# Performance work log

Measured on AMD Instinct MI355X. Metric: run time of the kernel, lower is better.

## Reference

```python
import jax, jax.numpy as jnp
import numpy as np

NUM_HEADS = 16
WINDOW_SIZE = 256  # config.window_size; layer is 'local'


def setup_inputs() -> dict:
    key = jax.random.key(0)
    ks = jax.random.split(key, 8)
    B, S, H = 4, 2048, 1024
    scale = 1.0 / np.sqrt(H)
    return {
        "x": jax.random.normal(ks[0], (B, S, H), dtype=jnp.float32),
        "x_clean": jax.random.normal(ks[1], (B, S, H), dtype=jnp.float32),
        "ablation_mask": jax.random.uniform(ks[2], (B, S, H), dtype=jnp.float32),
        "Wq": jax.random.normal(ks[3], (H, H), dtype=jnp.float32) * scale,
        "Wk": jax.random.normal(ks[4], (H, H), dtype=jnp.float32) * scale,
        "Wv": jax.random.normal(ks[5], (H, H), dtype=jnp.float32) * scale,
        "Wo": jax.random.normal(ks[6], (H, H), dtype=jnp.float32) * scale,
        "bo": jnp.zeros((H,), dtype=jnp.float32),
    }


def reference(x, x_clean, ablation_mask, Wq, Wk, Wv, Wo, bo):
    B, S, H = x.shape
    nh, hd = NUM_HEADS, H // NUM_HEADS

    def proj(inp, W):  # torch Linear: inp @ W.T -> split heads -> [B, nh, S, hd]
        return jnp.einsum('bsh,oh->bso', inp, W).reshape(B, S, nh, hd).transpose(0, 2, 1, 3)

    q = proj(x, Wq)
    k = proj(x_clean, Wk)
    v = proj(x_clean, Wv)

    # NOTE: original applies NO 1/sqrt(head_dim) scaling.
    scores = jnp.einsum('bnsd,bntd->bnst', q, k)  # [B, nh, S, S]

    i = jnp.arange(S)[:, None]
    j = jnp.arange(S)[None, :]
    # local mask: forbid future (j > i) OR too-far past (j <= i - window)
    masked = (j > i) | (j <= i - WINDOW_SIZE)
    scores = jnp.where(masked[None, None, :, :], -jnp.inf, scores)

    attn = jax.nn.softmax(scores, axis=-1)
    context = jnp.einsum('bnst,bntd->bnsd', attn, v)          # [B, nh, S, hd]
    context = context.transpose(0, 2, 1, 3).reshape(B, S, H)   # merge heads
    context = context * ablation_mask
    return jnp.einsum('bsh,oh->bso', context, Wo) + bo
```

## Files before the change

### kernel.cpp

```cpp
#include <hip/hip_runtime.h>
#include <hip/hip_bf16.h>
#include <cstddef>

#define SB 4
#define SS 2048
#define SH 1024
#define NH 16
#define HD 64
#define WIN 256

typedef __attribute__((ext_vector_type(8))) short bf16x8;
typedef __attribute__((ext_vector_type(8))) _Float16 f16x8;
typedef __attribute__((ext_vector_type(2))) __fp16 fp16v2;
typedef __attribute__((ext_vector_type(4))) float f32x4;

static __device__ __forceinline__ ushort2 pk_bf16(float a, float b) {
    __hip_bfloat162 h = __float22bfloat162_rn(make_float2(a, b));
    union { __hip_bfloat162 h2; ushort2 u2; } u;
    u.h2 = h;
    return u.u2;
}
static __device__ __forceinline__ unsigned short pk1(float a) {
    return pk_bf16(a, 0.f).x;
}

static __device__ __forceinline__ void async16(const void* gptr, void* lptr) {
    __builtin_amdgcn_global_load_lds(
        (const __attribute__((address_space(1))) unsigned int*)gptr,
        (__attribute__((address_space(3))) unsigned int*)lptr, 16, 0, 0);
}

#define CFENCE() asm volatile("" ::: "memory")

__global__ __launch_bounds__(256) void cvt_all(
    const float* __restrict__ x,  const float* __restrict__ xc,
    const float* __restrict__ Wq, const float* __restrict__ Wk,
    const float* __restrict__ Wv, const float* __restrict__ Wo,
    _Float16* __restrict__ xh,  _Float16* __restrict__ xch,
    _Float16* __restrict__ Wqh, _Float16* __restrict__ Wkh,
    _Float16* __restrict__ Wvh, _Float16* __restrict__ Woh)
{
    const int I4 = SB * SS * SH / 4;
    const int W4 = SH * SH / 4;
    int idx = blockIdx.x * 256 + threadIdx.x;
    const float* src;
    _Float16* dst;
    int off;
    if (idx < I4) { src = x; dst = xh; off = idx; }
    else if (idx < 2 * I4) { src = xc; dst = xch; off = idx - I4; }
    else {
        int r = idx - 2 * I4;
        int wi = r >> 18;
        off = r & (W4 - 1);
        src = (wi == 0) ? Wq : (wi == 1) ? Wk : (wi == 2) ? Wv : Wo;
        dst = (wi == 0) ? Wqh : (wi == 1) ? Wkh : (wi == 2) ? Wvh : Woh;
    }
    float4 v = ((const float4*)src)[off];
    union { fp16v2 h[2]; uint2 u; } t;
    t.h[0] = __builtin_amdgcn_cvt_pkrtz(v.x, v.y);
    t.h[1] = __builtin_amdgcn_cvt_pkrtz(v.z, v.w);
    ((uint2*)dst)[off] = t.u;
}

static __device__ __forceinline__ void gemm8_core(
    const _Float16* __restrict__ A, const _Float16* __restrict__ W,
    int m0, int n0, unsigned short* __restrict__ smem, f32x4 (&acc)[4][4])
{
    const int K = SH;
    const int NT = K / 64;
    const int tid = threadIdx.x;
    const int w = tid >> 6, lane = tid & 63;
    const int wm = (w >> 2) * 64;
    const int wn = (w & 3) * 64;
    const int lrow = lane & 15;
    const int lk8 = (lane >> 4) * 8;
    const int swz = (lrow & 7) << 3;

    const int srow = w * 8 + (lane >> 3);
    const int scol = ((lane & 7) ^ ((lane >> 3) & 7)) << 3;
    const _Float16* aS = A + (size_t)(m0 + srow) * K + scol;
    const _Float16* bS = W + (size_t)(n0 + srow) * K + scol;

    auto stA = [&](int tile, int half) {
        async16(aS + (size_t)(half * 64) * K + tile * 64,
                smem + ((tile & 1) << 13) + half * 4096 + w * 512);
    };
    auto stB = [&](int tile, int half) {
        async16(bS + (size_t)(half * 128) * K + tile * 64,
                smem + 16384 + ((tile & 1) << 14) + half * 8192 + w * 512);
        async16(bS + (size_t)(half * 128 + 64) * K + tile * 64,
                smem + 16384 + ((tile & 1) << 14) + half * 8192 + 4096 + w * 512);
    };

    f16x8 a[4][2];
    f16x8 b[2][2];

    stA(0, 0); stA(0, 1);
    stB(0, 0); stB(0, 1);
    stB(1, 0);
    asm volatile("s_waitcnt vmcnt(2)" ::: "memory");
    __builtin_amdgcn_s_barrier();
    CFENCE();

    for (int t = 0; t < NT; ++t) {
        const int cur = t & 1;
        unsigned short* LA = smem + (cur << 13);
        unsigned short* LB = smem + 16384 + (cur << 14);

#pragma unroll
        for (int m = 0; m < 4; ++m)
#pragma unroll
            for (int ks = 0; ks < 2; ++ks)
                a[m][ks] = *(const f16x8*)(LA + (wm + m * 16 + lrow) * 64 + ((ks * 32 + lk8) ^ swz));
#pragma unroll
        for (int n = 0; n < 2; ++n)
#pragma unroll
            for (int ks = 0; ks < 2; ++ks)
                b[n][ks] = *(const f16x8*)(LB + (wn + n * 16 + lrow) * 64 + ((ks * 32 + lk8) ^ swz));
        if (t + 1 < NT) { stA(t + 1, 0); stA(t + 1, 1); stB(t + 1, 1); }
        CFENCE();
        if (t + 1 < NT) asm volatile("s_waitcnt vmcnt(6)" ::: "memory");
        else            asm volatile("s_waitcnt vmcnt(0)" ::: "memory");
        __builtin_amdgcn_s_barrier();
        CFENCE();
        asm volatile("s_waitcnt lgkmcnt(0)" ::: "memory");
        __builtin_amdgcn_s_setprio(1);
#pragma unroll
        for (int ks = 0; ks < 2; ++ks)
#pragma unroll
            for (int m = 0; m < 4; ++m)
#pragma unroll
                for (int n = 0; n < 2; ++n)
                    acc[m][n] = __builtin_amdgcn_mfma_f32_16x16x32_f16(a[m][ks], b[n][ks], acc[m][n], 0, 0, 0);
        __builtin_amdgcn_s_setprio(0);
        CFENCE();
        __builtin_amdgcn_s_barrier();
        CFENCE();

#pragma unroll
        for (int n = 0; n < 2; ++n)
#pragma unroll
            for (int ks = 0; ks < 2; ++ks)
                b[n][ks] = *(const f16x8*)(LB + (wn + 32 + n * 16 + lrow) * 64 + ((ks * 32 + lk8) ^ swz));
        if (t + 2 < NT) stB(t + 2, 0);
        CFENCE();
        __builtin_amdgcn_s_barrier();
        CFENCE();
        asm volatile("s_waitcnt lgkmcnt(0)" ::: "memory");
        __builtin_amdgcn_s_setprio(1);
#pragma unroll
        for (int ks = 0; ks < 2; ++ks)
#pragma unroll
            for (int m = 0; m < 4; ++m)
#pragma unroll
                for (int n = 0; n < 2; ++n)
                    acc[m][2 + n] = __builtin_amdgcn_mfma_f32_16x16x32_f16(a[m][ks], b[n][ks], acc[m][2 + n], 0, 0, 0);
        __builtin_amdgcn_s_setprio(0);
        if (t < NT - 2)       asm volatile("s_waitcnt vmcnt(4)" ::: "memory");
        else if (t == NT - 2) asm volatile("s_waitcnt vmcnt(2)" ::: "memory");
        else                  asm volatile("s_waitcnt vmcnt(0)" ::: "memory");
        __builtin_amdgcn_s_barrier();
        CFENCE();
    }
    CFENCE();
}

__global__ __launch_bounds__(512, 2) void gemm_qkv8(
    const _Float16* __restrict__ xh, const _Float16* __restrict__ xch,
    const _Float16* __restrict__ Wqh, const _Float16* __restrict__ Wkh,
    const _Float16* __restrict__ Wvh,
    _Float16* __restrict__ Qh, _Float16* __restrict__ Kh,
    unsigned short* __restrict__ Vt)
{
    __shared__ __align__(16) unsigned short smem[49152];
    const int z = blockIdx.z;
    const _Float16* A = (z == 0) ? xh : xch;
    const _Float16* W = (z == 0) ? Wqh : (z == 1) ? Wkh : Wvh;
    const int m0 = blockIdx.x * 128;
    const int n0 = blockIdx.y * 256;

    f32x4 acc[4][4];
#pragma unroll
    for (int i = 0; i < 4; ++i)
#pragma unroll
        for (int j = 0; j < 4; ++j)
            acc[i][j] = (f32x4){0.f, 0.f, 0.f, 0.f};

    gemm8_core(A, W, m0, n0, smem, acc);

    const int tid = threadIdx.x;
    const int w = tid >> 6, lane = tid & 63;
    const int wm = (w >> 2) * 64, wn = (w & 3) * 64;
    const int lrow = lane & 15;
    const int rq = (lane >> 4) * 4;
    const int M = SB * SS, N = SH;

    if (z < 2) {
        _Float16* C = (z == 0) ? Qh : Kh;
        _Float16* T = (_Float16*)smem;
#pragma unroll
        for (int m = 0; m < 4; ++m)
#pragma unroll
            for (int n = 0; n < 4; ++n)
#pragma unroll
                for (int r = 0; r < 4; ++r)
                    T[(wm + m * 16 + rq + r) * 264 + wn + n * 16 + lrow] = (_Float16)acc[m][n][r];
        __syncthreads();
#pragma unroll
        for (int u = 0; u < 8; ++u) {
            int slot = u * 512 + tid;
            int row = slot >> 5;
            int c8 = (slot & 31) * 8;
            *(uint4*)(C + (size_t)(m0 + row) * N + n0 + c8) =
                *(const uint4*)&T[row * 264 + c8];
        }
    } else {
        unsigned short* T = smem;
#pragma unroll
        for (int n = 0; n < 4; ++n)
#pragma unroll
            for (int m = 0; m < 4; ++m) {
                int rt = wn + n * 16 + lrow;
                *(ushort4*)&T[rt * 136 + wm + m * 16 + rq] = make_ushort4(
                    pk1(acc[m][n][0]), pk1(acc[m][n][1]),
                    pk1(acc[m][n][2]), pk1(acc[m][n][3]));
            }
        __syncthreads();
#pragma unroll
        for (int u = 0; u < 8; ++u) {
            int slot = u * 512 + tid;
            int row = slot >> 4;
            int m8 = (slot & 15) * 8;
            *(uint4*)(Vt + (size_t)(n0 + row) * M + m0 + m8) =
                *(const uint4*)&T[row * 136 + m8];
        }
    }
}

__global__ __launch_bounds__(512, 2) void gemm_o8(
    const _Float16* __restrict__ A, const _Float16* __restrict__ W,
    const float* __restrict__ bias, float* __restrict__ C)
{
    __shared__ __align__(16) unsigned short smem[49152];
    const int m0 = blockIdx.x * 128;
    const int n0 = blockIdx.y * 256;

    f32x4 acc[4][4];
#pragma unroll
    for (int i = 0; i < 4; ++i)
#pragma unroll
        for (int j = 0; j < 4; ++j)
            acc[i][j] = (f32x4){0.f, 0.f, 0.f, 0.f};

    gemm8_core(A, W, m0, n0, smem, acc);

    const int tid = threadIdx.x;
    const int w = tid >> 6, lane = tid & 63;
    const int wm = (w >> 2) * 64, wn = (w & 3) * 64;
    const int lrow = lane & 15;
    const int rq = (lane >> 4) * 4;
    const int N = SH;

#pragma unroll
    for (int m = 0; m < 4; ++m) {
        int rbase = m0 + wm + m * 16 + rq;
#pragma unroll
        for (int n = 0; n < 4; ++n) {
            int col = n0 + wn + n * 16 + lrow;
            float badd = bias[col];
#pragma unroll
            for (int r = 0; r < 4; ++r)
                C[(size_t)(rbase + r) * N + col] = acc[m][n][r] + badd;
        }
    }
}

__global__ __launch_bounds__(512, 4) void attn5(
    const _Float16* Qg, const _Float16* __restrict__ Kg,
    const unsigned short* __restrict__ Vtg, const float* __restrict__ amask,
    _Float16* ctxg)
{
    __shared__ __align__(16) _Float16 K_s[2][64 * 64];
    __shared__ __align__(16) unsigned short V_s[2][64 * 64];
    __shared__ __align__(16) unsigned short P_s[8][32 * 72];

    const int t = threadIdx.x;
    const int wave = t >> 6, lane = t & 63;
    const int id = blockIdx.x;
    const int qb = id >> 6;
    const int pr = id & 63;
    const int h = pr & 15, b = pr >> 4;
    const int t0 = qb * 256;
    const int wq = t0 + wave * 32;
    const int lrow = lane & 15;
    const int lk8 = (lane >> 4) * 8;
    const int rq = (lane >> 4) * 4;
    const int M = SB * SS;
    unsigned short* P = P_s[wave];
    const int kswz = (lrow & 7) * 8;

    const int srow8 = lane >> 3;
    const int scol = ((lane & 7) ^ ((lane >> 3) & 7)) * 8;

    f16x8 qf[2][2];
#pragma unroll
    for (int i = 0; i < 2; ++i)
#pragma unroll
        for (int ki = 0; ki < 2; ++ki)
            qf[i][ki] = *(const f16x8*)(Qg +
                (size_t)(b * SS + wq + i * 16 + lrow) * SH + h * HD + ki * 32 + lk8);

    f32x4 o[2][4];
    float lsum[2][4];
#pragma unroll
    for (int i = 0; i < 2; ++i)
#pragma unroll
        for (int j = 0; j < 4; ++j) o[i][j] = (f32x4){0.f, 0.f, 0.f, 0.f};
#pragma unroll
    for (int i = 0; i < 2; ++i)
#pragma unroll
        for (int r = 0; r < 4; ++r) lsum[i][r] = 0.f;

    int cl0 = t0 - (WIN - 1);
    cl0 = cl0 < 0 ? 0 : cl0;
    const int c_lo = cl0 >> 6;
    const int c_hi = (t0 >> 6) + 3;

    auto stage = [&](int c, int buf) {
        const int key0 = c * 64;
        async16(Kg + (size_t)(b * SS + key0 + wave * 8 + srow8) * SH + h * HD + scol,
                (_Float16*)K_s[buf] + wave * 512);
        async16(Vtg + (size_t)(h * HD + wave * 8 + srow8) * M + b * SS + key0 + scol,
                (unsigned short*)V_s[buf] + wave * 512);
    };

    stage(c_lo, c_lo & 1);
    __syncthreads();

    for (int c = c_lo; c <= c_hi; ++c) {
        const int cur = c & 1;
        if (c < c_hi) stage(c + 1, cur ^ 1);
        const int key0 = c * 64;
        if (key0 <= wq + 31 && key0 + 63 >= wq - (WIN - 1)) {
            const _Float16* Kc = (const _Float16*)K_s[cur];
            const unsigned short* Vc = (const unsigned short*)V_s[cur];

            f32x4 s[2][4];
#pragma unroll
            for (int i = 0; i < 2; ++i)
#pragma unroll
                for (int j = 0; j < 4; ++j) s[i][j] = (f32x4){0.f, 0.f, 0.f, 0.f};
#pragma unroll
            for (int ki = 0; ki < 2; ++ki)
#pragma unroll
                for (int j = 0; j < 4; ++j) {
                    f16x8 bh = *(const f16x8*)&Kc[(j * 16 + lrow) * 64 + ((ki * 32 + lk8) ^ kswz)];
#pragma unroll
                    for (int i = 0; i < 2; ++i)
                        s[i][j] = __builtin_amdgcn_mfma_f32_16x16x32_f16(qf[i][ki], bh, s[i][j], 0, 0, 0);
                }

#pragma unroll
            for (int i = 0; i < 2; ++i)
#pragma unroll
                for (int j = 0; j < 4; ++j) {
                    int jg = key0 + j * 16 + lrow;
#pragma unroll
                    for (int r = 0; r < 4; ++r) {
                        int qg = wq + i * 16 + rq + r;
                        float p = (jg <= qg && jg > qg - WIN) ? __expf(s[i][j][r]) : 0.f;
                        lsum[i][r] += p;
                        P[(i * 16 + rq + r) * 72 + j * 16 + lrow] = pk1(p);
                    }
                }

#pragma unroll
            for (int ki = 0; ki < 2; ++ki) {
                bf16x8 pf[2];
#pragma unroll
                for (int i = 0; i < 2; ++i)
                    pf[i] = *(const bf16x8*)&P[(i * 16 + lrow) * 72 + ki * 32 + lk8];
#pragma unroll
                for (int j = 0; j < 4; ++j) {
                    bf16x8 vf = *(const bf16x8*)&Vc[(j * 16 + lrow) * 64 + ((ki * 32 + lk8) ^ kswz)];
#pragma unroll
                    for (int i = 0; i < 2; ++i)
                        o[i][j] = __builtin_amdgcn_mfma_f32_16x16x32_bf16(pf[i], vf, o[i][j], 0, 0, 0);
                }
            }
        }
        __syncthreads();
    }

#pragma unroll
    for (int i = 0; i < 2; ++i)
#pragma unroll
        for (int r = 0; r < 4; ++r) {
#pragma unroll
            for (int m = 1; m < 16; m <<= 1)
                lsum[i][r] += __shfl_xor(lsum[i][r], m);
        }

    _Float16* Pf = (_Float16*)P;
#pragma unroll
    for (int i = 0; i < 2; ++i)
#pragma unroll
        for (int r = 0; r < 4; ++r) {
            float inv = 1.f / lsum[i][r];
#pragma unroll
            for (int j = 0; j < 4; ++j)
                Pf[(i * 16 + rq + r) * 72 + j * 16 + lrow] = (_Float16)(o[i][j][r] * inv);
        }
#pragma unroll
    for (int u = 0; u < 4; ++u) {
        int slot = u * 64 + lane;
        int ro = slot >> 3;
        int d8 = (slot & 7) * 8;
        f16x8 v = *(const f16x8*)&Pf[ro * 72 + d8];
        size_t g = (size_t)(b * SS + wq + ro) * SH + h * HD + d8;
        float4 ma = *(const float4*)(amask + g);
        float4 mb = *(const float4*)(amask + g + 4);
        f16x8 rs;
        rs[0] = (_Float16)((float)v[0] * ma.x);
        rs[1] = (_Float16)((float)v[1] * ma.y);
        rs[2] = (_Float16)((float)v[2] * ma.z);
        rs[3] = (_Float16)((float)v[3] * ma.w);
        rs[4] = (_Float16)((float)v[4] * mb.x);
        rs[5] = (_Float16)((float)v[5] * mb.y);
        rs[6] = (_Float16)((float)v[6] * mb.z);
        rs[7] = (_Float16)((float)v[7] * mb.w);
        *(f16x8*)(ctxg + g) = rs;
    }
}

extern "C" void kernel_launch(void* const* d_in, const int* in_sizes, int n_in,
                              void* d_out, int out_size, void* d_ws, size_t ws_size,
                              hipStream_t stream)
{
    const float* x     = (const float*)d_in[0];
    const float* xc    = (const float*)d_in[1];
    const float* amask = (const float*)d_in[2];
    const float* Wq    = (const float*)d_in[3];
    const float* Wk    = (const float*)d_in[4];
    const float* Wv    = (const float*)d_in[5];
    const float* Wo    = (const float*)d_in[6];
    const float* bo    = (const float*)d_in[7];
    float* out = (float*)d_out;

    const int M = SB * SS;
    const size_t BUF = (size_t)M * SH;
    const size_t WBUF = (size_t)SH * SH;
    _Float16* xh  = (_Float16*)d_ws;
    _Float16* xch = xh + BUF;
    _Float16* Qh  = xch + BUF;
    _Float16* Kh  = Qh + BUF;
    unsigned short* Vt = (unsigned short*)(Kh + BUF);
    _Float16* Wqh = (_Float16*)(Vt + BUF);
    _Float16* Wkh = Wqh + WBUF;
    _Float16* Wvh = Wkh + WBUF;
    _Float16* Woh = Wvh + WBUF;
    _Float16* ctx = Qh;

    const int total4 = 2 * (M * SH / 4) + 4 * (SH * SH / 4);
    hipLaunchKernelGGL(cvt_all, dim3(total4 / 256), dim3(256), 0, stream,
                       x, xc, Wq, Wk, Wv, Wo, xh, xch, Wqh, Wkh, Wvh, Woh);

    hipLaunchKernelGGL(gemm_qkv8, dim3(M / 128, SH / 256, 3), dim3(512), 0, stream,
                       xh, xch, Wqh, Wkh, Wvh, Qh, Kh, Vt);

    hipLaunchKernelGGL(attn5, dim3((SS / 256) * NH * SB), dim3(512), 0, stream,
                       Qh, Kh, Vt, amask, ctx);

    hipLaunchKernelGGL(gemm_o8, dim3(M / 128, SH / 256), dim3(512), 0, stream,
                       ctx, Woh, bo, out);
}
```

Before: 271.7 us.

## Fuse fp32-to-fp16 conversion of activations into QKV GEMM A-tile loading

The separate conversion pass over x and x_clean is removed; the QKV GEMM now loads fp32 A tiles into registers, converts them to fp16 and writes them swizzled into LDS, while B still streams through async global-to-LDS loads. This drops a full read/write pass over two 32 MB activation tensors plus the fp16 round trip. In exchange the GEMM reads twice the A bytes (fp32), and each of the four N-blocks rereads and reconverts the same A rows. The register-staged A path also adds VGPR pressure and hand-tuned waitcnt bookkeeping.

```diff
diff --git a/kernel.cpp b/kernel.cpp
--- a/kernel.cpp
+++ b/kernel.cpp
@@ -23,6 +23,11 @@
 static __device__ __forceinline__ unsigned short pk1(float a) {
     return pk_bf16(a, 0.f).x;
 }
+static __device__ __forceinline__ unsigned pk2u(float a, float b) {
+    union { fp16v2 h; unsigned u; } v;
+    v.h = __builtin_amdgcn_cvt_pkrtz(a, b);
+    return v.u;
+}
 
 static __device__ __forceinline__ void async16(const void* gptr, void* lptr) {
     __builtin_amdgcn_global_load_lds(
@@ -32,34 +37,147 @@
 
 #define CFENCE() asm volatile("" ::: "memory")
 
-__global__ __launch_bounds__(256) void cvt_all(
-    const float* __restrict__ x,  const float* __restrict__ xc,
+__global__ __launch_bounds__(256) void cvt_w(
     const float* __restrict__ Wq, const float* __restrict__ Wk,
     const float* __restrict__ Wv, const float* __restrict__ Wo,
-    _Float16* __restrict__ xh,  _Float16* __restrict__ xch,
     _Float16* __restrict__ Wqh, _Float16* __restrict__ Wkh,
     _Float16* __restrict__ Wvh, _Float16* __restrict__ Woh)
 {
-    const int I4 = SB * SS * SH / 4;
     const int W4 = SH * SH / 4;
     int idx = blockIdx.x * 256 + threadIdx.x;
-    const float* src;
-    _Float16* dst;
-    int off;
-    if (idx < I4) { src = x; dst = xh; off = idx; }
-    else if (idx < 2 * I4) { src = xc; dst = xch; off = idx - I4; }
-    else {
-        int r = idx - 2 * I4;
-        int wi = r >> 18;
-        off = r & (W4 - 1);
-        src = (wi == 0) ? Wq : (wi == 1) ? Wk : (wi == 2) ? Wv : Wo;
-        dst = (wi == 0) ? Wqh : (wi == 1) ? Wkh : (wi == 2) ? Wvh : Woh;
+    int wi = idx >> 18;
+    int off = idx & (W4 - 1);
+    const float* src = (wi == 0) ? Wq : (wi == 1) ? Wk : (wi == 2) ? Wv : Wo;
+    _Float16* dst = (wi == 0) ? Wqh : (wi == 1) ? Wkh : (wi == 2) ? Wvh : Woh;
+    float4 v = ((const float4*)src)[off];
+    uint2 t;
+    t.x = pk2u(v.x, v.y);
+    t.y = pk2u(v.z, v.w);
+    ((uint2*)dst)[off] = t;
+}
+
+static __device__ __forceinline__ void gemm8_core_f32a(
+    const float* __restrict__ A, const _Float16* __restrict__ W,
+    int m0, int n0, unsigned short* __restrict__ smem, f32x4 (&acc)[4][4])
+{
+    const int K = SH;
+    const int NT = K / 64;
+    const int tid = threadIdx.x;
+    const int w = tid >> 6, lane = tid & 63;
+    const int wm = (w >> 2) * 64;
+    const int wn = (w & 3) * 64;
+    const int lrow = lane & 15;
+    const int lk8 = (lane >> 4) * 8;
+    const int swz = (lrow & 7) << 3;
+
+    const int srow = w * 8 + (lane >> 3);
+    const int scol = ((lane & 7) ^ ((lane >> 3) & 7)) << 3;
+    const _Float16* bS = W + (size_t)(n0 + srow) * K + scol;
+
+    auto stB = [&](int tile, int half) {
+        async16(bS + (size_t)(half * 128) * K + tile * 64,
+                smem + 16384 + ((tile & 1) << 14) + half * 8192 + w * 512);
+        async16(bS + (size_t)(half * 128 + 64) * K + tile * 64,
+                smem + 16384 + ((tile & 1) << 14) + half * 8192 + 4096 + w * 512);
+    };
+
+    const int r = tid >> 2;
+    const int cg = (tid & 3) * 16;
+    const int s0 = ((tid & 3) * 2) ^ (r & 7);
+    const float* aF = A + (size_t)(m0 + r) * K + cg;
+
+    float4 L0, L1, L2, L3;
+    auto loadA = [&](int tile) {
+        const float4* p = (const float4*)(aF + tile * 64);
+        L0 = p[0]; L1 = p[1]; L2 = p[2]; L3 = p[3];
+    };
+    auto writeA = [&](int tile) {
+        unsigned short* dst = smem + ((tile & 1) << 13) + r * 64;
+        uint4 w0, w1;
+        w0.x = pk2u(L0.x, L0.y); w0.y = pk2u(L0.z, L0.w);
+        w0.z = pk2u(L1.x, L1.y); w0.w = pk2u(L1.z, L1.w);
+        w1.x = pk2u(L2.x, L2.y); w1.y = pk2u(L2.z, L2.w);
+        w1.z = pk2u(L3.x, L3.y); w1.w = pk2u(L3.z, L3.w);
+        *(uint4*)&dst[s0 * 8] = w0;
+        *(uint4*)&dst[(s0 ^ 1) * 8] = w1;
+    };
+
+    f16x8 a[4][2];
+    f16x8 b[2][2];
+
+    loadA(0);
+    stB(0, 0); stB(0, 1); stB(1, 0);
+    asm volatile("s_waitcnt vmcnt(6)" ::: "memory");
+    writeA(0);
+    loadA(1);
+    asm volatile("s_waitcnt vmcnt(6)" ::: "memory");
+    asm volatile("s_waitcnt lgkmcnt(0)" ::: "memory");
+    __builtin_amdgcn_s_barrier();
+    CFENCE();
+
+    for (int t = 0; t < NT; ++t) {
+        const int cur = t & 1;
+        unsigned short* LA = smem + (cur << 13);
+        unsigned short* LB = smem + 16384 + (cur << 14);
+
+#pragma unroll
+        for (int m = 0; m < 4; ++m)
+#pragma unroll
+            for (int ks = 0; ks < 2; ++ks)
+                a[m][ks] = *(const f16x8*)(LA + (wm + m * 16 + lrow) * 64 + ((ks * 32 + lk8) ^ swz));
+#pragma unroll
+        for (int n = 0; n < 2; ++n)
+#pragma unroll
+            for (int ks = 0; ks < 2; ++ks)
+                b[n][ks] = *(const f16x8*)(LB + (wn + n * 16 + lrow) * 64 + ((ks * 32 + lk8) ^ swz));
+        if (t + 1 < NT) stB(t + 1, 1);
+        CFENCE();
+        if (t + 1 < NT) asm volatile("s_waitcnt vmcnt(8)" ::: "memory");
+        else            asm volatile("s_waitcnt vmcnt(0)" ::: "memory");
+        __builtin_amdgcn_s_barrier();
+        CFENCE();
+        asm volatile("s_waitcnt lgkmcnt(0)" ::: "memory");
+        __builtin_amdgcn_s_setprio(1);
+#pragma unroll
+        for (int ks = 0; ks < 2; ++ks)
+#pragma unroll
+            for (int m = 0; m < 4; ++m)
+#pragma unroll
+                for (int n = 0; n < 2; ++n)
+                    acc[m][n] = __builtin_amdgcn_mfma_f32_16x16x32_f16(a[m][ks], b[n][ks], acc[m][n], 0, 0, 0);
+        __builtin_amdgcn_s_setprio(0);
+        CFENCE();
+        __builtin_amdgcn_s_barrier();
+        CFENCE();
+
+#pragma unroll
+        for (int n = 0; n < 2; ++n)
+#pragma unroll
+            for (int ks = 0; ks < 2; ++ks)
+                b[n][ks] = *(const f16x8*)(LB + (wn + 32 + n * 16 + lrow) * 64 + ((ks * 32 + lk8) ^ swz));
+        if (t + 1 < NT) {
+            asm volatile("s_waitcnt vmcnt(2)" ::: "memory");
+            writeA(t + 1);
+        }
+        if (t + 2 < NT) { stB(t + 2, 0); loadA(t + 2); }
+        CFENCE();
+        __builtin_amdgcn_s_barrier();
+        CFENCE();
+        asm volatile("s_waitcnt lgkmcnt(0)" ::: "memory");
+        __builtin_amdgcn_s_setprio(1);
+#pragma unroll
+        for (int ks = 0; ks < 2; ++ks)
+#pragma unroll
+            for (int m = 0; m < 4; ++m)
+#pragma unroll
+                for (int n = 0; n < 2; ++n)
+                    acc[m][2 + n] = __builtin_amdgcn_mfma_f32_16x16x32_f16(a[m][ks], b[n][ks], acc[m][2 + n], 0, 0, 0);
+        __builtin_amdgcn_s_setprio(0);
+        CFENCE();
+        __builtin_amdgcn_s_barrier();
+        CFENCE();
     }
-    float4 v = ((const float4*)src)[off];
-    union { fp16v2 h[2]; uint2 u; } t;
-    t.h[0] = __builtin_amdgcn_cvt_pkrtz(v.x, v.y);
-    t.h[1] = __builtin_amdgcn_cvt_pkrtz(v.z, v.w);
-    ((uint2*)dst)[off] = t.u;
+    CFENCE();
 }
 
 static __device__ __forceinline__ void gemm8_core(
@@ -166,7 +284,7 @@
 }
 
 __global__ __launch_bounds__(512, 2) void gemm_qkv8(
-    const _Float16* __restrict__ xh, const _Float16* __restrict__ xch,
+    const float* __restrict__ x, const float* __restrict__ xc,
     const _Float16* __restrict__ Wqh, const _Float16* __restrict__ Wkh,
     const _Float16* __restrict__ Wvh,
     _Float16* __restrict__ Qh, _Float16* __restrict__ Kh,
@@ -174,7 +292,7 @@
 {
     __shared__ __align__(16) unsigned short smem[49152];
     const int z = blockIdx.z;
-    const _Float16* A = (z == 0) ? xh : xch;
+    const float* A = (z == 0) ? x : xc;
     const _Float16* W = (z == 0) ? Wqh : (z == 1) ? Wkh : Wvh;
     const int m0 = blockIdx.x * 128;
     const int n0 = blockIdx.y * 256;
@@ -186,7 +304,7 @@
         for (int j = 0; j < 4; ++j)
             acc[i][j] = (f32x4){0.f, 0.f, 0.f, 0.f};
 
-    gemm8_core(A, W, m0, n0, smem, acc);
+    gemm8_core_f32a(A, W, m0, n0, smem, acc);
 
     const int tid = threadIdx.x;
     const int w = tid >> 6, lane = tid & 63;
@@ -461,12 +579,11 @@
     _Float16* Woh = Wvh + WBUF;
     _Float16* ctx = Qh;
 
-    const int total4 = 2 * (M * SH / 4) + 4 * (SH * SH / 4);
-    hipLaunchKernelGGL(cvt_all, dim3(total4 / 256), dim3(256), 0, stream,
-                       x, xc, Wq, Wk, Wv, Wo, xh, xch, Wqh, Wkh, Wvh, Woh);
+    hipLaunchKernelGGL(cvt_w, dim3(4 * (SH * SH / 4) / 256), dim3(256), 0, stream,
+                       Wq, Wk, Wv, Wo, Wqh, Wkh, Wvh, Woh);
 
     hipLaunchKernelGGL(gemm_qkv8, dim3(M / 128, SH / 256, 3), dim3(512), 0, stream,
-                       xh, xch, Wqh, Wkh, Wvh, Qh, Kh, Vt);
+                       x, xc, Wqh, Wkh, Wvh, Qh, Kh, Vt);
 
     hipLaunchKernelGGL(attn5, dim3((SS / 256) * NH * SB), dim3(512), 0, stream,
                        Qh, Kh, Vt, amask, ctx);
```

New measurement: 275.5 us. No clear change (+1.4%).
